# Kernel optimization log

Hardware: AMD Instinct MI355X
Metric: run time of the kernel (lower is better)

Reference implementation:

```python
import jax, jax.numpy as jnp
import numpy as np

B, A, D = 1024, 200, 128
H = 8
DH = D // H
TANH_CLIP = 10.0


def setup_inputs() -> dict:
    key = jax.random.key(0)
    k = jax.random.split(key, 8)
    agent_embd = jax.random.normal(k[0], (B, A, D), dtype=jnp.float32)
    # old_action must be a permutation per row (no revisits under the mask)
    old_action = jax.vmap(lambda kk: jax.random.permutation(kk, A))(
        jax.random.split(k[1], B)).astype(jnp.int32)
    s = 0.02
    W_placeholder = jax.random.uniform(k[2], (D,), jnp.float32, -1.0, 1.0)
    W_node = jax.random.normal(k[3], (D, 3 * D), jnp.float32) * s   # project_node_embeddings
    W_fixed = jax.random.normal(k[4], (D, D), jnp.float32) * s      # project_fixed_context
    W_step = jax.random.normal(k[5], (D, D), jnp.float32) * s       # project_step_context
    W_out = jax.random.normal(k[6], (D, D), jnp.float32) * s        # project_out
    return {"agent_embd": agent_embd, "old_action": old_action,
            "W_placeholder": W_placeholder, "W_node": W_node,
            "W_fixed": W_fixed, "W_step": W_step, "W_out": W_out}


def _decode(agent_embd, old_action, W_placeholder, W_node, W_fixed, W_step, W_out):
    b_, a_, d_ = agent_embd.shape
    inv_sqrt_dh = np.float32(1.0 / np.sqrt(DH))
    inv_sqrt_d = np.float32(1.0 / np.sqrt(d_))
    batch_ix = jnp.arange(b_)

    # _precompute: fixed context + per-head K/V + logit keys
    graph_embed = agent_embd.mean(axis=1)                      # [B, D]
    fixed_ctx = graph_embed @ W_fixed                          # [B, D]
    proj = agent_embd @ W_node                                 # [B, A, 3D]
    gK, gV, logit_K = jnp.split(proj, 3, axis=-1)              # each [B, A, D]
    gK = gK.reshape(b_, a_, H, DH).transpose(2, 0, 1, 3)       # [H, B, A, dh]
    gV = gV.reshape(b_, a_, H, DH).transpose(2, 0, 1, 3)       # [H, B, A, dh]

    def step(carry, xs):
        mask, prev = carry                                     # [B, A] bool, [B] int
        i, act = xs
        gathered = agent_embd[batch_ix, prev]                  # [B, D]
        step_ctx = jnp.where(i == 0, W_placeholder[None, :], gathered)
        query = fixed_ctx + step_ctx @ W_step                  # [B, D]
        mask = jnp.where(i > 0, mask.at[batch_ix, prev].set(True), mask)

        Q = query.reshape(b_, H, DH).transpose(1, 0, 2)        # [H, B, dh]
        compat = jnp.einsum('hbd,hbad->hba', Q, gK) * inv_sqrt_dh
        compat = jnp.where(mask[None, :, :], -jnp.inf, compat)  # mask_inner
        attn = jax.nn.softmax(compat, axis=-1)                 # [H, B, A]
        heads = jnp.einsum('hba,hbad->hbd', attn, gV)          # [H, B, dh]
        glimpse = heads.transpose(1, 0, 2).reshape(b_, d_) @ W_out  # [B, D]

        logits = jnp.einsum('bd,bad->ba', glimpse, logit_K) * inv_sqrt_d
        logits = jnp.tanh(logits) * TANH_CLIP
        logits = jnp.where(mask, -jnp.inf, logits)             # mask_logits
        log_p = jax.nn.log_softmax(logits, axis=-1)            # [B, A]
        lp_sel = log_p[batch_ix, act]                          # [B]
        return (mask, act), lp_sel

    mask0 = jnp.zeros((b_, a_), dtype=bool)
    prev0 = jnp.zeros((b_,), dtype=old_action.dtype)
    xs = (jnp.arange(a_), old_action.T)
    _, lps = jax.lax.scan(step, (mask0, prev0), xs)            # lps: [A, B]
    return old_action, lps.sum(axis=0)


def reference(agent_embd, old_action, W_placeholder, W_node, W_fixed, W_step, W_out):
    return _decode(agent_embd, old_action, W_placeholder, W_node, W_fixed, W_step, W_out)
```

## Files before the change

### kernel.cpp

```cpp
#include <hip/hip_runtime.h>
#include <cstdint>
#include <cstddef>

#define BB 1024
#define AA 200
#define DD 128
#define HH 8
#define N3 384

typedef unsigned short u16;
typedef unsigned int u32;
typedef __attribute__((ext_vector_type(8))) short bf16x8;
typedef __attribute__((ext_vector_type(4))) float f32x4;

__device__ __forceinline__ float bf2f(u16 v){ return __uint_as_float(((u32)v) << 16); }
__device__ __forceinline__ u16 f2bf(float f){
  u32 u = __float_as_uint(f);
  u32 r = u + 0x7fffu + ((u >> 16) & 1u);
  return (u16)(r >> 16);
}
__device__ __forceinline__ u32 pack2(float lo, float hi){
  return (u32)f2bf(lo) | ((u32)f2bf(hi) << 16);
}
__device__ __forceinline__ u32 pack2t(float lo, float hi){
  return (__float_as_uint(hi) & 0xFFFF0000u) | (__float_as_uint(lo) >> 16);
}
__device__ __forceinline__ bf16x8 pack8(float4 a, float4 b){
  bf16x8 o;
  o[0] = (short)f2bf(a.x); o[1] = (short)f2bf(a.y);
  o[2] = (short)f2bf(a.z); o[3] = (short)f2bf(a.w);
  o[4] = (short)f2bf(b.x); o[5] = (short)f2bf(b.y);
  o[6] = (short)f2bf(b.z); o[7] = (short)f2bf(b.w);
  return o;
}

__global__ void k_act_rank(const int* __restrict__ oa, float* __restrict__ out0,
                           int* __restrict__ rank){
  int m = blockIdx.x * 256 + threadIdx.x;
  if (m >= BB*AA) return;
  int v = oa[m];
  out0[m] = (float)v;
  int b = m / AA;
  int j = m - b*AA;
  rank[b*AA + v] = j;
}

__global__ void k_prep(const float* __restrict__ Wn, const float* __restrict__ Ws,
                       const float* __restrict__ Wo,
                       u16* __restrict__ WnT, u16* __restrict__ WsT,
                       u16* __restrict__ WoT){
  int idx = blockIdx.x * 256 + threadIdx.x;
  if (idx < 49152){
    int n = idx >> 7, k = idx & 127;
    WnT[idx] = f2bf(Wn[k*N3 + n]);
  } else if (idx < 65536){
    int j = idx - 49152;
    int n = j >> 7, k = j & 127;
    WsT[j] = f2bf(Ws[k*DD + n]);
  } else if (idx < 81920){
    int j = idx - 65536;
    int n = j >> 7, k = j & 127;
    WoT[j] = f2bf(Wo[k*DD + n]);
  }
}

__global__ void k_fixed(const float* __restrict__ E, const float* __restrict__ Wf,
                        float* __restrict__ fixedc){
  int b = blockIdx.x;
  int t = threadIdx.x;
  int half = t >> 7, d = t & 127;
  __shared__ float ge[2][DD];
  const float* Eb = E + (size_t)b*AA*DD + (size_t)half*100*DD;
  float s = 0.f;
  #pragma unroll 4
  for (int a = 0; a < 100; ++a) s += Eb[a*DD + d];
  ge[half][d] = s;
  __syncthreads();
  if (t < DD){
    float g = (ge[0][t] + ge[1][t]) * (1.0f/AA);
    float acc = 0.f;
    for (int k = 0; k < DD; ++k){
      float gk = (ge[0][k] + ge[1][k]) * (1.0f/AA);
      acc = fmaf(gk, Wf[k*DD + t], acc);
    }
    (void)g;
    fixedc[b*DD + t] = acc;
  }
}

__global__ __launch_bounds__(256) void k_proj_mfma(const float* __restrict__ E,
                                                   const u16* __restrict__ WnT,
                                                   u16* __restrict__ proj){
  const int t = threadIdx.x;
  const int w = t >> 6, L = t & 63;
  const int l16 = L & 15, lq = L >> 4;
  const int row = blockIdx.x * 64 + w*16 + l16;
  const float* Erow = E + (size_t)row*DD;
  u16* dst = proj + (size_t)row*N3;

  #pragma unroll
  for (int c = 0; c < 3; ++c){
    const int n0 = c*128;
    f32x4 acc[8] = {};
    #pragma unroll
    for (int ks = 0; ks < 4; ++ks){
      int ko = ks*32 + lq*8;
      bf16x8 bfrag = pack8(*(const float4*)(Erow + ko), *(const float4*)(Erow + ko + 4));
      #pragma unroll
      for (int nt = 0; nt < 8; ++nt){
        union { uint4 u; bf16x8 v; } aa;
        aa.u = *(const uint4*)(WnT + (size_t)(n0 + nt*16 + l16)*DD + ko);
        acc[nt] = __builtin_amdgcn_mfma_f32_16x16x32_bf16(aa.v, bfrag, acc[nt], 0, 0, 0);
      }
    }
    #pragma unroll
    for (int nt = 0; nt < 8; ++nt){
      uint2 ov;
      ov.x = pack2(acc[nt][0], acc[nt][1]);
      ov.y = pack2(acc[nt][2], acc[nt][3]);
      *(uint2*)(dst + n0 + nt*16 + lq*4) = ov;
    }
  }
}

__global__ __launch_bounds__(256) void k_query_mfma(const float* __restrict__ E,
                                                    const int* __restrict__ oa,
                                                    const float* __restrict__ Wp,
                                                    const u16* __restrict__ WsT,
                                                    const float* __restrict__ fixedc,
                                                    u16* __restrict__ qhg){
  const int t = threadIdx.x;
  const int w = t >> 6, L = t & 63;
  const int l16 = L & 15, lq = L >> 4;
  const int m0 = blockIdx.x * 128;
  const int row0 = m0 + w*32;

  const float* src[2];
  #pragma unroll
  for (int mt = 0; mt < 2; ++mt){
    int q = row0 + mt*16 + l16;
    int b = q / AA, i = q - b*AA;
    src[mt] = (i == 0) ? Wp : (E + (size_t)(b*AA + oa[b*AA + i - 1])*DD);
  }

  f32x4 acc[2][8] = {};
  #pragma unroll
  for (int ks = 0; ks < 4; ++ks){
    int ko = ks*32 + lq*8;
    bf16x8 a0 = pack8(*(const float4*)(src[0] + ko), *(const float4*)(src[0] + ko + 4));
    bf16x8 a1 = pack8(*(const float4*)(src[1] + ko), *(const float4*)(src[1] + ko + 4));
    #pragma unroll
    for (int nt = 0; nt < 8; ++nt){
      union { uint4 u; bf16x8 v; } bb;
      bb.u = *(const uint4*)(WsT + (size_t)(nt*16 + l16)*DD + ko);
      acc[0][nt] = __builtin_amdgcn_mfma_f32_16x16x32_bf16(a0, bb.v, acc[0][nt], 0, 0, 0);
      acc[1][nt] = __builtin_amdgcn_mfma_f32_16x16x32_bf16(a1, bb.v, acc[1][nt], 0, 0, 0);
    }
  }
  #pragma unroll
  for (int mt = 0; mt < 2; ++mt)
    #pragma unroll
    for (int r = 0; r < 4; ++r){
      int row = row0 + mt*16 + lq*4 + r;
      int b = row / AA;
      const float* fc = fixedc + (size_t)b*DD;
      u16* dst = qhg + (size_t)row*DD;
      #pragma unroll
      for (int nt = 0; nt < 8; ++nt)
        dst[nt*16 + l16] = f2bf((acc[mt][nt][r] + fc[nt*16 + l16]) * 0.25f);
    }
}

#define KSTR 24
#define VSTR 232
template<int IT>
__device__ __forceinline__ void attn_tile(const u16* KL, const u16* VT,
                                          u16* Qbase, int l16, int lq,
                                          bool dm0, bool dm1, bool dm2, bool dm3){
  constexpr int NT = 13 - IT;
  const int qi = IT*16 + l16;
  const float NEG_INF = -__builtin_inff();

  union { uint4 u; bf16x8 v; } qf8;
  qf8.u.x = 0; qf8.u.y = 0; qf8.u.z = 0; qf8.u.w = 0;
  if (qi < AA){
    uint2 q2 = *(const uint2*)(Qbase + (size_t)qi*DD + lq*4);
    qf8.u.x = q2.x; qf8.u.y = q2.y;
  }

  f32x4 S[NT];
  #pragma unroll
  for (int k = 0; k < NT; ++k){
    const int at = IT + k;
    union { uint4 u; bf16x8 v; } kf8;
    uint2 k2 = *(const uint2*)&KL[(at*16 + l16)*KSTR + lq*4];
    kf8.u.x = k2.x; kf8.u.y = k2.y; kf8.u.z = 0; kf8.u.w = 0;
    f32x4 z = {0.f,0.f,0.f,0.f};
    S[k] = __builtin_amdgcn_mfma_f32_16x16x32_bf16(kf8.v, qf8.v, z, 0, 0, 0);
  }
  S[0][0] = dm0 ? NEG_INF : S[0][0];
  S[0][1] = dm1 ? NEG_INF : S[0][1];
  S[0][2] = dm2 ? NEG_INF : S[0][2];
  S[0][3] = dm3 ? NEG_INF : S[0][3];
  if (lq >= 2){
    S[NT-1][0] = NEG_INF; S[NT-1][1] = NEG_INF;
    S[NT-1][2] = NEG_INF; S[NT-1][3] = NEG_INF;
  }
  float m = fmaxf(fmaxf(S[0][0], S[0][1]), fmaxf(S[0][2], S[0][3]));
  #pragma unroll
  for (int k = 1; k < NT; ++k)
    m = fmaxf(m, fmaxf(fmaxf(S[k][0], S[k][1]), fmaxf(S[k][2], S[k][3])));
  m = fmaxf(m, __shfl_xor(m, 16));
  m = fmaxf(m, __shfl_xor(m, 32));
  m = fmaxf(m, -1e30f);
  float s0 = 0.f, s1 = 0.f, s2 = 0.f, s3 = 0.f;
  #pragma unroll
  for (int k = 0; k < NT; ++k){
    float e0 = __expf(S[k][0] - m);
    float e1 = __expf(S[k][1] - m);
    float e2 = __expf(S[k][2] - m);
    float e3 = __expf(S[k][3] - m);
    S[k][0] = e0; S[k][1] = e1; S[k][2] = e2; S[k][3] = e3;
    s0 += e0; s1 += e1; s2 += e2; s3 += e3;
  }
  float sum = (s0 + s1) + (s2 + s3);
  sum += __shfl_xor(sum, 16);
  sum += __shfl_xor(sum, 32);
  float inv = 1.0f / sum;
  f32x4 acc = {0.f,0.f,0.f,0.f};
  #pragma unroll
  for (int k = 0; k < NT; ++k){
    const int at = IT + k;
    union { uint4 u; bf16x8 v; } pa8, vb8;
    pa8.u.x = pack2t(S[k][0], S[k][1]);
    pa8.u.y = pack2t(S[k][2], S[k][3]);
    pa8.u.z = 0; pa8.u.w = 0;
    uint2 v2 = *(const uint2*)&VT[l16*VSTR + at*16 + lq*4];
    vb8.u.x = v2.x; vb8.u.y = v2.y; vb8.u.z = 0; vb8.u.w = 0;
    acc = __builtin_amdgcn_mfma_f32_16x16x32_bf16(vb8.v, pa8.v, acc, 0, 0, 0);
  }
  if (qi < AA){
    uint2 ov;
    ov.x = pack2(acc[0]*inv, acc[1]*inv);
    ov.y = pack2(acc[2]*inv, acc[3]*inv);
    *(uint2*)(Qbase + (size_t)qi*DD + lq*4) = ov;
  }
}

__global__ __launch_bounds__(256) void k_attn(const u16* __restrict__ proj,
                                              const int* __restrict__ oa,
                                              u16* __restrict__ qhg){
  __shared__ __align__(16) u16 KL[208*KSTR];
  __shared__ __align__(16) u16 VT[16*VSTR];
  const int b = blockIdx.x;
  const int h = blockIdx.y;
  const int t = threadIdx.x;
  const int w = t >> 6, L = t & 63;
  const int l16 = L & 15, lq = L >> 4;

  if (t < 192) KL[200*KSTR + t] = 0;
  if (t < 128){ int d = t >> 3, c = t & 7; VT[d*VSTR + 200 + c] = 0; }

  if (t < AA){
    int a = oa[(size_t)b*AA + t];
    const u16* src = proj + ((size_t)(b*AA + a))*N3 + h*16;
    uint4 k0 = *(const uint4*)(src);
    uint4 k1 = *(const uint4*)(src + 8);
    *(uint4*)&KL[t*KSTR]     = k0;
    *(uint4*)&KL[t*KSTR + 8] = k1;
    const u16* sv = src + 128;
    u16 d16[16];
    *(uint4*)(d16)   = *(const uint4*)(sv);
    *(uint4*)(d16+8) = *(const uint4*)(sv+8);
    #pragma unroll
    for (int d = 0; d < 16; ++d) VT[d*VSTR + t] = d16[d];
  }
  __syncthreads();

  u16* Qbase = qhg + (size_t)b*AA*DD + h*16;
  const bool dm0 = (lq*4 + 0) < l16;
  const bool dm1 = (lq*4 + 1) < l16;
  const bool dm2 = (lq*4 + 2) < l16;
  const bool dm3 = (lq*4 + 3) < l16;

  if (w == 0){
    attn_tile<0>(KL, VT, Qbase, l16, lq, dm0, dm1, dm2, dm3);
    attn_tile<3>(KL, VT, Qbase, l16, lq, dm0, dm1, dm2, dm3);
  } else if (w == 1){
    attn_tile<1>(KL, VT, Qbase, l16, lq, dm0, dm1, dm2, dm3);
    attn_tile<2>(KL, VT, Qbase, l16, lq, dm0, dm1, dm2, dm3);
  } else if (w == 2){
    attn_tile<4>(KL, VT, Qbase, l16, lq, dm0, dm1, dm2, dm3);
    attn_tile<6>(KL, VT, Qbase, l16, lq, dm0, dm1, dm2, dm3);
    attn_tile<8>(KL, VT, Qbase, l16, lq, dm0, dm1, dm2, dm3);
    attn_tile<10>(KL, VT, Qbase, l16, lq, dm0, dm1, dm2, dm3);
    attn_tile<12>(KL, VT, Qbase, l16, lq, dm0, dm1, dm2, dm3);
  } else {
    attn_tile<5>(KL, VT, Qbase, l16, lq, dm0, dm1, dm2, dm3);
    attn_tile<7>(KL, VT, Qbase, l16, lq, dm0, dm1, dm2, dm3);
    attn_tile<9>(KL, VT, Qbase, l16, lq, dm0, dm1, dm2, dm3);
    attn_tile<11>(KL, VT, Qbase, l16, lq, dm0, dm1, dm2, dm3);
  }
}

__global__ __launch_bounds__(256) void k_glimpse_mfma(const u16* __restrict__ qhg,
                                                      const u16* __restrict__ WoT,
                                                      u16* __restrict__ proj){
  const int t = threadIdx.x;
  const int w = t >> 6, L = t & 63;
  const int l16 = L & 15, lq = L >> 4;
  const int m0 = blockIdx.x * 128;
  const int row0 = m0 + w*32;

  f32x4 acc[2][8] = {};
  const u16* Arow0 = qhg + (size_t)(row0 + l16)*DD;
  const u16* Arow1 = Arow0 + (size_t)16*DD;
  #pragma unroll
  for (int ks = 0; ks < 4; ++ks){
    int ko = ks*32 + lq*8;
    union { uint4 u; bf16x8 v; } a0, a1;
    a0.u = *(const uint4*)(Arow0 + ko);
    a1.u = *(const uint4*)(Arow1 + ko);
    #pragma unroll
    for (int nt = 0; nt < 8; ++nt){
      union { uint4 u; bf16x8 v; } bb;
      bb.u = *(const uint4*)(WoT + (size_t)(nt*16 + l16)*DD + ko);
      acc[0][nt] = __builtin_amdgcn_mfma_f32_16x16x32_bf16(a0.v, bb.v, acc[0][nt], 0, 0, 0);
      acc[1][nt] = __builtin_amdgcn_mfma_f32_16x16x32_bf16(a1.v, bb.v, acc[1][nt], 0, 0, 0);
    }
  }
  #pragma unroll
  for (int mt = 0; mt < 2; ++mt)
    #pragma unroll
    for (int r = 0; r < 4; ++r){
      int row = row0 + mt*16 + lq*4 + r;
      u16* dst = proj + (size_t)row*N3;
      #pragma unroll
      for (int nt = 0; nt < 8; ++nt)
        dst[nt*16 + l16] = f2bf(acc[mt][nt][r]);
    }
}

__global__ __launch_bounds__(256) void k_logits(const u16* __restrict__ proj,
                                                const int* __restrict__ rank,
                                                const int* __restrict__ oa,
                                                float* __restrict__ outlps){
  __shared__ float red[4];
  const int b = blockIdx.x;
  const int t = threadIdx.x;
  const int w = t >> 6, L = t & 63;
  const int l16 = L & 15, lq = L >> 4;
  const float inv_sqrt_d = 0.08838834764831843f;

  const u16* Gbase  = proj + (size_t)b*AA*N3;
  const u16* LKbase = Gbase + 256;

  int ra[13];
  #pragma unroll
  for (int at = 0; at < 13; ++at){
    int a = at*16 + l16;
    ra[at] = (a < AA) ? rank[b*AA + a] : -1;
  }

  float lp_part = 0.f;

  for (int it = w; it < 13; it += 4){
    bf16x8 af[4];
    {
      const u16* arow = Gbase + (size_t)(it*16 + l16)*N3;
      #pragma unroll
      for (int kb = 0; kb < 4; ++kb){
        union { uint4 u; bf16x8 v; } tmp;
        tmp.u = *(const uint4*)(arow + kb*32 + lq*8);
        af[kb] = tmp.v;
      }
    }
    f32x4 S[13];
    #pragma unroll
    for (int at = 0; at < 13; ++at){
      const u16* brow = LKbase + (size_t)(at*16 + l16)*N3;
      f32x4 acc = {0.f,0.f,0.f,0.f};
      #pragma unroll
      for (int kb = 0; kb < 4; ++kb){
        union { uint4 u; bf16x8 v; } tmp;
        tmp.u = *(const uint4*)(brow + kb*32 + lq*8);
        acc = __builtin_amdgcn_mfma_f32_16x16x32_bf16(af[kb], tmp.v, acc, 0, 0, 0);
      }
      S[at] = acc;
    }
    #pragma unroll
    for (int at = 0; at < 13; ++at)
      #pragma unroll
      for (int r = 0; r < 4; ++r){
        int i = it*16 + lq*4 + r;
        float x = S[at][r] * inv_sqrt_d;
        float e = __expf(2.0f*x);
        float th = 1.0f - 2.0f/(e + 1.0f);
        S[at][r] = (ra[at] < i) ? -__builtin_inff() : 10.0f*th;
      }
    #pragma unroll
    for (int r = 0; r < 4; ++r){
      int i = it*16 + lq*4 + r;
      float m = S[0][r];
      #pragma unroll
      for (int at = 1; at < 13; ++at) m = fmaxf(m, S[at][r]);
      #pragma unroll
      for (int off = 1; off < 16; off <<= 1) m = fmaxf(m, __shfl_xor(m, off));
      float sum = 0.f;
      #pragma unroll
      for (int at = 0; at < 13; ++at) sum += __expf(S[at][r] - m);
      #pragma unroll
      for (int off = 1; off < 16; off <<= 1) sum += __shfl_xor(sum, off);
      if (i < AA){
        float lse = m + __logf(sum);
        int act = oa[b*AA + i];
        if ((act & 15) == l16){
          int at0 = act >> 4;
          #pragma unroll
          for (int at = 0; at < 13; ++at)
            if (at == at0) lp_part += S[at][r] - lse;
        }
      }
    }
  }
  #pragma unroll
  for (int off = 1; off < 64; off <<= 1) lp_part += __shfl_xor(lp_part, off);
  if (L == 0) red[w] = lp_part;
  __syncthreads();
  if (t == 0) outlps[b] = red[0] + red[1] + red[2] + red[3];
}

extern "C" void kernel_launch(void* const* d_in, const int* in_sizes, int n_in,
                              void* d_out, int out_size, void* d_ws, size_t ws_size,
                              hipStream_t stream){
  const float* E  = (const float*)d_in[0];
  const int*   oa = (const int*)d_in[1];
  const float* Wp = (const float*)d_in[2];
  const float* Wn = (const float*)d_in[3];
  const float* Wf = (const float*)d_in[4];
  const float* Ws = (const float*)d_in[5];
  const float* Wo = (const float*)d_in[6];
  float* out = (float*)d_out;

  char* ws = (char*)d_ws;
  int*   rank   = (int*)ws;
  float* fixedc = (float*)(ws + 819200);
  u16*   proj   = (u16*)(ws + 1343488);
  u16*   qhg    = (u16*)(ws + 158629888);
  u16*   WnT    = (u16*)(ws + 211058688);
  u16*   WsT    = (u16*)(ws + 211156992);
  u16*   WoT    = (u16*)(ws + 211189760);

  k_act_rank<<<dim3((BB*AA)/256), 256, 0, stream>>>(oa, out, rank);
  k_prep<<<dim3(320), 256, 0, stream>>>(Wn, Ws, Wo, WnT, WsT, WoT);
  k_fixed<<<dim3(BB), 256, 0, stream>>>(E, Wf, fixedc);
  k_proj_mfma<<<dim3((BB*AA)/64), 256, 0, stream>>>(E, WnT, proj);
  k_query_mfma<<<dim3((BB*AA)/128), 256, 0, stream>>>(E, oa, Wp, WsT, fixedc, qhg);
  k_attn<<<dim3(BB, HH), 256, 0, stream>>>(proj, oa, qhg);
  k_glimpse_mfma<<<dim3((BB*AA)/128), 256, 0, stream>>>(qhg, WoT, proj);
  k_logits<<<dim3(BB), 256, 0, stream>>>(proj, rank, oa, out + BB*AA);
}
```

Measured before the change: 726.8 us.

## Stage projection input tile in swizzled LDS and remap attention block order

The node projection kernel now loads a 128-row tile of the embeddings into LDS as bf16 with an XOR swizzle. Each wave computes two 16-row MFMA tiles, so every weight fragment load is reused twice and the grid is halved. The output store changes from packed uint2 writes to scalar 16-bit stores, which may cost write bandwidth. The attention kernel uses a 1D grid with a remapped batch/head index, presumably to improve L2/cache locality across heads of the same batch.

Result: faster. 635.4 us (-12.6%).

```diff
diff --git a/kernel.cpp b/kernel.cpp
--- a/kernel.cpp
+++ b/kernel.cpp
@@ -77,13 +77,11 @@
   ge[half][d] = s;
   __syncthreads();
   if (t < DD){
-    float g = (ge[0][t] + ge[1][t]) * (1.0f/AA);
     float acc = 0.f;
     for (int k = 0; k < DD; ++k){
       float gk = (ge[0][k] + ge[1][k]) * (1.0f/AA);
       acc = fmaf(gk, Wf[k*DD + t], acc);
     }
-    (void)g;
     fixedc[b*DD + t] = acc;
   }
 }
@@ -91,35 +89,57 @@
 __global__ __launch_bounds__(256) void k_proj_mfma(const float* __restrict__ E,
                                                    const u16* __restrict__ WnT,
                                                    u16* __restrict__ proj){
+  __shared__ __align__(16) u16 EL[128*128];
   const int t = threadIdx.x;
   const int w = t >> 6, L = t & 63;
   const int l16 = L & 15, lq = L >> 4;
-  const int row = blockIdx.x * 64 + w*16 + l16;
-  const float* Erow = E + (size_t)row*DD;
-  u16* dst = proj + (size_t)row*N3;
+  const int m0 = blockIdx.x * 128;
+
+  const float4* Ef4 = (const float4*)(E + (size_t)m0*DD);
+  #pragma unroll
+  for (int i = 0; i < 16; ++i){
+    int v = i*256 + t;
+    int row = v >> 5, c4 = v & 31;
+    float4 f = Ef4[v];
+    uint2 p; p.x = pack2(f.x, f.y); p.y = pack2(f.z, f.w);
+    int byte_off = (row << 8) + ((c4 << 3) ^ ((row & 7) << 4));
+    *(uint2*)((char*)EL + byte_off) = p;
+  }
+  __syncthreads();
+
+  const int r0 = w*32 + l16;
+  const int r1 = r0 + 16;
+  const int sw = (l16 & 7) << 4;
 
   #pragma unroll
   for (int c = 0; c < 3; ++c){
     const int n0 = c*128;
-    f32x4 acc[8] = {};
+    f32x4 acc[2][8] = {};
     #pragma unroll
     for (int ks = 0; ks < 4; ++ks){
-      int ko = ks*32 + lq*8;
-      bf16x8 bfrag = pack8(*(const float4*)(Erow + ko), *(const float4*)(Erow + ko + 4));
+      const int kb = ks*64 + lq*16;
+      const int ko = ks*32 + lq*8;
+      union { uint4 u; bf16x8 v; } a0, a1;
+      a0.u = *(const uint4*)((const char*)EL + (r0 << 8) + (kb ^ sw));
+      a1.u = *(const uint4*)((const char*)EL + (r1 << 8) + (kb ^ sw));
       #pragma unroll
       for (int nt = 0; nt < 8; ++nt){
-        union { uint4 u; bf16x8 v; } aa;
-        aa.u = *(const uint4*)(WnT + (size_t)(n0 + nt*16 + l16)*DD + ko);
-        acc[nt] = __builtin_amdgcn_mfma_f32_16x16x32_bf16(aa.v, bfrag, acc[nt], 0, 0, 0);
-      }
-    }
-    #pragma unroll
-    for (int nt = 0; nt < 8; ++nt){
-      uint2 ov;
-      ov.x = pack2(acc[nt][0], acc[nt][1]);
-      ov.y = pack2(acc[nt][2], acc[nt][3]);
-      *(uint2*)(dst + n0 + nt*16 + lq*4) = ov;
-    }
+        union { uint4 u; bf16x8 v; } bb;
+        bb.u = *(const uint4*)(WnT + (size_t)(n0 + nt*16 + l16)*DD + ko);
+        acc[0][nt] = __builtin_amdgcn_mfma_f32_16x16x32_bf16(a0.v, bb.v, acc[0][nt], 0, 0, 0);
+        acc[1][nt] = __builtin_amdgcn_mfma_f32_16x16x32_bf16(a1.v, bb.v, acc[1][nt], 0, 0, 0);
+      }
+    }
+    #pragma unroll
+    for (int mt = 0; mt < 2; ++mt)
+      #pragma unroll
+      for (int r = 0; r < 4; ++r){
+        int row = m0 + w*32 + mt*16 + lq*4 + r;
+        u16* dst = proj + (size_t)row*N3 + n0;
+        #pragma unroll
+        for (int nt = 0; nt < 8; ++nt)
+          dst[nt*16 + l16] = f2bf(acc[mt][nt][r]);
+      }
   }
 }
 
@@ -252,8 +272,9 @@
                                               u16* __restrict__ qhg){
   __shared__ __align__(16) u16 KL[208*KSTR];
   __shared__ __align__(16) u16 VT[16*VSTR];
-  const int b = blockIdx.x;
-  const int h = blockIdx.y;
+  const int idx = blockIdx.x;
+  const int b = ((idx & 7) << 7) + (idx >> 6);
+  const int h = (idx >> 3) & 7;
   const int t = threadIdx.x;
   const int w = t >> 6, L = t & 63;
   const int l16 = L & 15, lq = L >> 4;
@@ -454,9 +475,9 @@
   k_act_rank<<<dim3((BB*AA)/256), 256, 0, stream>>>(oa, out, rank);
   k_prep<<<dim3(320), 256, 0, stream>>>(Wn, Ws, Wo, WnT, WsT, WoT);
   k_fixed<<<dim3(BB), 256, 0, stream>>>(E, Wf, fixedc);
-  k_proj_mfma<<<dim3((BB*AA)/64), 256, 0, stream>>>(E, WnT, proj);
+  k_proj_mfma<<<dim3((BB*AA)/128), 256, 0, stream>>>(E, WnT, proj);
   k_query_mfma<<<dim3((BB*AA)/128), 256, 0, stream>>>(E, oa, Wp, WsT, fixedc, qhg);
-  k_attn<<<dim3(BB, HH), 256, 0, stream>>>(proj, oa, qhg);
+  k_attn<<<dim3(BB*HH), 256, 0, stream>>>(proj, oa, qhg);
   k_glimpse_mfma<<<dim3((BB*AA)/128), 256, 0, stream>>>(qhg, WoT, proj);
   k_logits<<<dim3(BB), 256, 0, stream>>>(proj, rank, oa, out + BB*AA);
 }
```
